# Performance work log

Hardware: AMD Instinct MI355X
Metric: run time of the kernel (lower is better)

## Reference

```python
import jax, jax.numpy as jnp
import numpy as np

B, S, D, H, DH = 8, 2048, 1024, 16, 64  # hidden_dim = H*DH


def _layer_norm(x, g, b, eps=1e-5):
    m = jnp.mean(x, axis=-1, keepdims=True)
    v = jnp.mean((x - m) ** 2, axis=-1, keepdims=True)
    return (x - m) / jnp.sqrt(v + eps) * g + b


def setup_inputs() -> dict:
    key = jax.random.key(0)
    ks = jax.random.split(key, 12)
    def xav(k, shape):
        # xavier_uniform with gain for relu = sqrt(2)
        fan_in, fan_out = shape[0], shape[1]
        a = np.sqrt(2.0) * np.sqrt(6.0 / (fan_in + fan_out))
        return jax.random.uniform(k, shape, jnp.float32, -a, a)
    return {
        "input_Q": jax.random.normal(ks[0], (B, S, D), jnp.float32),
        "input_K": jax.random.normal(ks[1], (B, S, D), jnp.float32),
        "input_V": jax.random.normal(ks[2], (B, S, D), jnp.float32),
        # weights stored [in, out] (torch Linear weight transposed)
        "Wq1": xav(ks[3], (D, DH // 2)),
        "Wq2": xav(ks[4], (DH // 2, DH * H)),
        "Wk1": xav(ks[5], (D, DH // 2)),
        "Wk2": xav(ks[6], (DH // 2, DH * H)),
        "Wv": xav(ks[7], (D, DH * H)),
        "Wfc": xav(ks[8], (D, D)),
        "A": xav(ks[9], (DH, DH)),
        "ln_g": jnp.ones((D,), jnp.float32),
        "ln_b": jnp.zeros((D,), jnp.float32),
    }


def reference(input_Q, input_K, input_V, Wq1, Wq2, Wk1, Wk2, Wv, Wfc, A, ln_g, ln_b):
    b, s, d = input_Q.shape
    residual = input_Q
    Q = (input_Q @ Wq1 @ Wq2).reshape(b, s, H, DH).transpose(0, 2, 1, 3)  # [B,H,S,dh]
    K = (input_K @ Wk1 @ Wk2).reshape(b, s, H, DH).transpose(0, 2, 1, 3)
    V = (input_V @ Wv).reshape(b, s, H, DH).transpose(0, 2, 1, 3)
    scale = 1.0 / np.sqrt(DH).astype(np.float32)
    # stage 1: scores[b,h,d,s] = sum_f A.T[d,f] K[b,h,s,f]
    scores_VV = jnp.einsum('fd,bhsf->bhds', A, K) * scale  # [B,H,dh,S]
    attn_VV = jax.nn.softmax(scores_VV, axis=-1)
    VV = jnp.einsum('bhds,bhsf->bhdf', attn_VV, V)  # [B,H,dh,dh]
    # stage 2: scores2[b,h,s,d] = sum_f Q[b,h,s,f] A[d,f]
    scores_VV2 = jnp.einsum('bhsf,df->bhsd', Q, A) * scale  # [B,H,S,dh]
    attn_VV2 = jax.nn.softmax(scores_VV2, axis=-1)
    VVV = jnp.einsum('bhsd,bhdf->bhsf', attn_VV2, VV)  # [B,H,S,dh]
    # faithful torch reshape: row-major flatten of [B,H,S,dh] into [B,S,H*dh]
    VVV = VVV.reshape(b, s, H * DH)
    outputs1 = _layer_norm(VVV + residual, ln_g, ln_b)
    outputs2 = outputs1 @ Wfc
    outputs = _layer_norm(outputs2 + outputs1, ln_g, ln_b)
    return (outputs, attn_VV)
```

## Files before the change

kernel.cpp:

```cpp
#include <hip/hip_runtime.h>
#include <hip/hip_bf16.h>
#include <stdint.h>

typedef __attribute__((ext_vector_type(4))) float f32x4;
typedef __attribute__((ext_vector_type(8))) short bf16x8;
typedef __attribute__((ext_vector_type(4))) unsigned short us4;
typedef __attribute__((ext_vector_type(8))) unsigned short us8;

static constexpr int Bb = 8, Ss = 2048, Dd = 1024, Hh = 16, DHh = 64;
static constexpr int Mm = Bb * Ss;
#define DEVI static __device__ __forceinline__

DEVI float bf2f(unsigned short u) {
  union { unsigned int i; float f; } v; v.i = ((unsigned int)u) << 16; return v.f;
}
DEVI unsigned short f2bf(float f) {
  union { float f; unsigned int i; } v; v.f = f;
  unsigned int r = v.i + 0x7FFFu + ((v.i >> 16) & 1u);
  return (unsigned short)(r >> 16);
}

__global__ __launch_bounds__(256) void k_transpose_w(const float* __restrict__ W,
                                                     unsigned short* __restrict__ WT) {
  __shared__ float tile[32][33];
  const int n0 = blockIdx.x * 32, k0 = blockIdx.y * 32;
  const int t = threadIdx.x, tr = t >> 5, tc = t & 31;
#pragma unroll
  for (int i = 0; i < 4; i++) {
    int r = tr + 8 * i;
    tile[r][tc] = W[(size_t)(k0 + r) * 1024 + n0 + tc];
  }
  __syncthreads();
#pragma unroll
  for (int i = 0; i < 4; i++) {
    int r = tr + 8 * i;
    WT[(size_t)(n0 + r) * 1024 + k0 + tc] = f2bf(tile[tc][r]);
  }
}

__global__ __launch_bounds__(256) void k_cvt(const float* __restrict__ x,
                                             unsigned short* __restrict__ y) {
  const int n4 = (Mm * Dd) / 4;
  for (int i = blockIdx.x * 256 + threadIdx.x; i < n4; i += gridDim.x * 256) {
    f32x4 v = ((const f32x4*)x)[i];
    us4 o = { f2bf(v.x), f2bf(v.y), f2bf(v.z), f2bf(v.w) };
    ((us4*)y)[i] = o;
  }
}

__global__ __launch_bounds__(256) void k_prep_at(const float* __restrict__ A,
                                                 unsigned short* __restrict__ At,
                                                 unsigned short* __restrict__ Ab) {
  int t = blockIdx.x * 256 + threadIdx.x;
  int d = t >> 6, f = t & 63;
  At[d * 64 + f] = f2bf(A[f * 64 + d]);
  Ab[t] = f2bf(A[t]);
}

__global__ __launch_bounds__(256) void k_qkmid(const float* __restrict__ inQ, const float* __restrict__ inK,
                                               const float* __restrict__ Wq1, const float* __restrict__ Wk1,
                                               float* __restrict__ Qmid, float* __restrict__ Kmid) {
  const float* in = blockIdx.y ? inK : inQ;
  const float* W  = blockIdx.y ? Wk1 : Wq1;
  float* outp     = blockIdx.y ? Kmid : Qmid;
  __shared__ float rows[8][1024];
  const int r0 = blockIdx.x * 8;
  const int t = threadIdx.x;
  const f32x4* src = (const f32x4*)(in + (size_t)r0 * 1024);
  f32x4* dstl = (f32x4*)rows;
#pragma unroll
  for (int i = 0; i < 8; i++) dstl[t + 256 * i] = src[t + 256 * i];
  __syncthreads();
  const int g = t >> 5, j = t & 31;
  float acc = 0.f;
#pragma unroll 8
  for (int k = 0; k < 1024; k++) acc += rows[g][k] * W[k * 32 + j];
  outp[(size_t)(r0 + g) * 32 + j] = acc;
}

__global__ __launch_bounds__(256) void k_qkexpand(const float* __restrict__ Qmid, const float* __restrict__ Kmid,
                                                  const float* __restrict__ Wq2, const float* __restrict__ Wk2,
                                                  unsigned short* __restrict__ Qp, unsigned short* __restrict__ Kp) {
  const float* mid = blockIdx.y ? Kmid : Qmid;
  const float* W   = blockIdx.y ? Wk2 : Wq2;
  unsigned short* outp = blockIdx.y ? Kp : Qp;
  __shared__ float sv[16][32];
  const int r0 = blockIdx.x * 16;
  const int t = threadIdx.x;
  ((float*)sv)[t]       = mid[(size_t)r0 * 32 + t];
  ((float*)sv)[t + 256] = mid[(size_t)r0 * 32 + t + 256];
  __syncthreads();
  const int c0 = t * 4;
  f32x4 acc[16];
#pragma unroll
  for (int ri = 0; ri < 16; ri++) acc[ri] = (f32x4){0.f, 0.f, 0.f, 0.f};
#pragma unroll
  for (int k = 0; k < 32; k++) {
    f32x4 w = *(const f32x4*)&W[k * 1024 + c0];
#pragma unroll
    for (int ri = 0; ri < 16; ri++) acc[ri] += sv[ri][k] * w;
  }
  const int h = c0 >> 6, f = c0 & 63;
#pragma unroll
  for (int ri = 0; ri < 16; ri++) {
    int r = r0 + ri;
    int b = r >> 11, s = r & 2047;
    us4 o = { f2bf(acc[ri].x), f2bf(acc[ri].y), f2bf(acc[ri].z), f2bf(acc[ri].w) };
    *(us4*)&outp[(((size_t)(b * 16 + h) * 2048) + s) * 64 + f] = o;
  }
}

__global__ __launch_bounds__(256) void k_transpose_bh(const unsigned short* __restrict__ src,
                                                      unsigned short* __restrict__ dst) {
  __shared__ unsigned short tile[64][72];
  const int bh = blockIdx.y, s0 = blockIdx.x * 64;
  const int t = threadIdx.x;
  {
    int sl = t >> 2, fc = (t & 3) * 16;
    const unsigned short* sp = src + ((size_t)bh * 2048 + s0 + sl) * 64 + fc;
    *(us8*)&tile[sl][fc]     = *(const us8*)sp;
    *(us8*)&tile[sl][fc + 8] = *(const us8*)(sp + 8);
  }
  __syncthreads();
  {
    int f = t >> 2, sc = (t & 3) * 16;
    unsigned short* dp = dst + ((size_t)bh * 64 + f) * 2048 + s0 + sc;
    us8 a, bq;
#pragma unroll
    for (int i = 0; i < 8; i++) a[i] = tile[sc + i][f];
#pragma unroll
    for (int i = 0; i < 8; i++) bq[i] = tile[sc + 8 + i][f];
    *(us8*)dp = a;
    *(us8*)(dp + 8) = bq;
  }
}

template <int EPI>
__global__ __launch_bounds__(256) void k_gemm(const unsigned short* __restrict__ Ag,
                                              const unsigned short* __restrict__ BTg,
                                              void* __restrict__ Cout) {
  __shared__ unsigned short As[128 * 64];
  __shared__ unsigned short Bs[128 * 64];
  const int m0 = blockIdx.y * 128, n0 = blockIdx.x * 128;
  const int t = threadIdx.x;
  const int w = t >> 6, l = t & 63;
  const int wr = w >> 1, wc = w & 1;
  const int g4 = l >> 4, l16 = l & 15;
  f32x4 acc[4][4];
#pragma unroll
  for (int i = 0; i < 4; i++)
#pragma unroll
    for (int jj = 0; jj < 4; jj++) acc[i][jj] = (f32x4){0.f, 0.f, 0.f, 0.f};

  const int srow = t >> 1, shalf = (t & 1) * 32;
  const us8* ga = (const us8*)(Ag  + (size_t)(m0 + srow) * 1024 + shalf);
  const us8* gb = (const us8*)(BTg + (size_t)(n0 + srow) * 1024 + shalf);
  const int swz = (srow & 7) << 4;
#pragma unroll 1
  for (int kt = 0; kt < 16; kt++) {
    __syncthreads();
#pragma unroll
    for (int c = 0; c < 4; c++) {
      int kb = (shalf + c * 8) * 2;
      *(us8*)&As[srow * 64 + ((kb ^ swz) >> 1)] = ga[c];
      *(us8*)&Bs[srow * 64 + ((kb ^ swz) >> 1)] = gb[c];
    }
    ga += 8; gb += 8;
    __syncthreads();
#pragma unroll
    for (int kk = 0; kk < 64; kk += 32) {
      bf16x8 af[4], bfr[4];
      const int kbyte = (kk + 8 * g4) * 2;
#pragma unroll
      for (int mt = 0; mt < 4; mt++) {
        int row = wr * 64 + mt * 16 + l16;
        af[mt] = *(const bf16x8*)&As[row * 64 + ((kbyte ^ ((row & 7) << 4)) >> 1)];
      }
#pragma unroll
      for (int nt = 0; nt < 4; nt++) {
        int row = wc * 64 + nt * 16 + l16;
        bfr[nt] = *(const bf16x8*)&Bs[row * 64 + ((kbyte ^ ((row & 7) << 4)) >> 1)];
      }
#pragma unroll
      for (int mt = 0; mt < 4; mt++)
#pragma unroll
        for (int nt = 0; nt < 4; nt++)
          acc[mt][nt] = __builtin_amdgcn_mfma_f32_16x16x32_bf16(af[mt], bfr[nt], acc[mt][nt], 0, 0, 0);
    }
  }
#pragma unroll
  for (int mt = 0; mt < 4; mt++)
#pragma unroll
    for (int nt = 0; nt < 4; nt++)
#pragma unroll
      for (int r = 0; r < 4; r++) {
        int m = m0 + wr * 64 + mt * 16 + g4 * 4 + r;
        int n = n0 + wc * 64 + nt * 16 + l16;
        float v = acc[mt][nt][r];
        if (EPI == 0) {
          int b = m >> 11, s = m & 2047, h = n >> 6, f = n & 63;
          ((unsigned short*)Cout)[(((size_t)(b * 16 + h) * 2048) + s) * 64 + f] = f2bf(v);
        } else {
          ((float*)Cout)[(size_t)m * 1024 + n] = v;
        }
      }
}

__global__ __launch_bounds__(512) void k_stage1m(const unsigned short* __restrict__ Kp,
                                                 const unsigned short* __restrict__ VpT,
                                                 const unsigned short* __restrict__ At,
                                                 float* __restrict__ attn_out,
                                                 float* __restrict__ VVn) {
  __shared__ unsigned short Ks[256 * 64];
  __shared__ unsigned short VTs[64 * 256];
  __shared__ unsigned short Ps[64 * 256];
  __shared__ float mred[512], lred[512], mfin[64], linv[64];
  const int bh = blockIdx.x;
  const int t = threadIdx.x;
  const int w = t >> 6, l = t & 63;
  const int l16 = l & 15, g4 = l >> 4;
  const unsigned short* kg = Kp  + (size_t)bh * 131072;
  const unsigned short* vg = VpT + (size_t)bh * 131072;

  bf16x8 bfr[4][2];
#pragma unroll
  for (int nt = 0; nt < 4; nt++)
#pragma unroll
    for (int ks = 0; ks < 2; ks++)
      bfr[nt][ks] = *(const bf16x8*)&At[(nt * 16 + l16) * 64 + ks * 32 + g4 * 8];

  float m4[4], l4[4];
#pragma unroll
  for (int nt = 0; nt < 4; nt++) { m4[nt] = -1e30f; l4[nt] = 0.f; }

  for (int st = 0; st < 8; st++) {
    __syncthreads();
#pragma unroll
    for (int i = 0; i < 4; i++) {
      int chunk = t + 512 * i;
      int row = chunk >> 3, fo = (chunk & 7) * 8;
      us8 v = *(const us8*)&kg[(size_t)(st * 256 + row) * 64 + fo];
      *(us8*)&Ks[row * 64 + (((fo * 2) ^ ((row & 7) << 4)) >> 1)] = v;
    }
    __syncthreads();
    f32x4 s_[2][4];
#pragma unroll
    for (int mt = 0; mt < 2; mt++)
#pragma unroll
      for (int nt = 0; nt < 4; nt++) s_[mt][nt] = (f32x4){0.f, 0.f, 0.f, 0.f};
#pragma unroll
    for (int mt = 0; mt < 2; mt++) {
      int ar = w * 32 + mt * 16 + l16;
#pragma unroll
      for (int ks = 0; ks < 2; ks++) {
        bf16x8 af = *(const bf16x8*)&Ks[ar * 64 + (((ks * 64 + g4 * 16) ^ ((ar & 7) << 4)) >> 1)];
#pragma unroll
        for (int nt = 0; nt < 4; nt++)
          s_[mt][nt] = __builtin_amdgcn_mfma_f32_16x16x32_bf16(af, bfr[nt][ks], s_[mt][nt], 0, 0, 0);
      }
    }
#pragma unroll
    for (int nt = 0; nt < 4; nt++) {
      float tm = s_[0][nt][0];
#pragma unroll
      for (int r = 1; r < 4; r++) tm = fmaxf(tm, s_[0][nt][r]);
#pragma unroll
      for (int r = 0; r < 4; r++) tm = fmaxf(tm, s_[1][nt][r]);
      tm *= 0.125f;
      float mn = fmaxf(m4[nt], tm);
      float sum = 0.f;
#pragma unroll
      for (int mt = 0; mt < 2; mt++)
#pragma unroll
        for (int r = 0; r < 4; r++) sum += __expf(s_[mt][nt][r] * 0.125f - mn);
      l4[nt] = l4[nt] * __expf(m4[nt] - mn) + sum;
      m4[nt] = mn;
    }
  }
#pragma unroll
  for (int nt = 0; nt < 4; nt++) {
#pragma unroll
    for (int off = 16; off < 64; off <<= 1) {
      float m2 = __shfl_xor(m4[nt], off);
      float l2 = __shfl_xor(l4[nt], off);
      float mn = fmaxf(m4[nt], m2);
      l4[nt] = l4[nt] * __expf(m4[nt] - mn) + l2 * __expf(m2 - mn);
      m4[nt] = mn;
    }
  }
  if (l < 16) {
#pragma unroll
    for (int nt = 0; nt < 4; nt++) {
      mred[w * 64 + nt * 16 + l] = m4[nt];
      lred[w * 64 + nt * 16 + l] = l4[nt];
    }
  }
  __syncthreads();
  if (w == 0) {
    float m = -1e30f;
#pragma unroll
    for (int wv = 0; wv < 8; wv++) m = fmaxf(m, mred[wv * 64 + l]);
    float ls = 0.f;
#pragma unroll
    for (int wv = 0; wv < 8; wv++) ls += lred[wv * 64 + l] * __expf(mred[wv * 64 + l] - m);
    mfin[l] = m;
    linv[l] = 1.f / ls;
  }

  f32x4 vv[2];
  vv[0] = (f32x4){0.f, 0.f, 0.f, 0.f};
  vv[1] = (f32x4){0.f, 0.f, 0.f, 0.f};
  const int mtv = w & 3, nbase = (w >> 2) * 2;
  float* aout = attn_out + (size_t)bh * 131072;
  for (int st = 0; st < 8; st++) {
    __syncthreads();
#pragma unroll
    for (int i = 0; i < 4; i++) {
      int chunk = t + 512 * i;
      {
        int row = chunk >> 3, fo = (chunk & 7) * 8;
        us8 v = *(const us8*)&kg[(size_t)(st * 256 + row) * 64 + fo];
        *(us8*)&Ks[row * 64 + (((fo * 2) ^ ((row & 7) << 4)) >> 1)] = v;
      }
      {
        int fr = chunk >> 5, so = (chunk & 31) * 8;
        us8 v = *(const us8*)&vg[(size_t)fr * 2048 + st * 256 + so];
        *(us8*)&VTs[fr * 256 + (((so * 2) ^ ((fr & 7) << 4)) >> 1)] = v;
      }
    }
    __syncthreads();
    f32x4 s_[2][4];
#pragma unroll
    for (int mt = 0; mt < 2; mt++)
#pragma unroll
      for (int nt = 0; nt < 4; nt++) s_[mt][nt] = (f32x4){0.f, 0.f, 0.f, 0.f};
#pragma unroll
    for (int mt = 0; mt < 2; mt++) {
      int ar = w * 32 + mt * 16 + l16;
#pragma unroll
      for (int ks = 0; ks < 2; ks++) {
        bf16x8 af = *(const bf16x8*)&Ks[ar * 64 + (((ks * 64 + g4 * 16) ^ ((ar & 7) << 4)) >> 1)];
#pragma unroll
        for (int nt = 0; nt < 4; nt++)
          s_[mt][nt] = __builtin_amdgcn_mfma_f32_16x16x32_bf16(af, bfr[nt][ks], s_[mt][nt], 0, 0, 0);
      }
    }
#pragma unroll
    for (int mt = 0; mt < 2; mt++) {
      int sg = w * 32 + mt * 16 + g4 * 4;
#pragma unroll
      for (int nt = 0; nt < 4; nt++) {
        int d = nt * 16 + l16;
        float mf = mfin[d], il = linv[d];
        f32x4 ev;
#pragma unroll
        for (int r = 0; r < 4; r++) ev[r] = __expf(s_[mt][nt][r] * 0.125f - mf);
        f32x4 av = ev * il;
        *(f32x4*)&aout[(size_t)d * 2048 + st * 256 + sg] = av;
        us4 pb = { f2bf(ev.x), f2bf(ev.y), f2bf(ev.z), f2bf(ev.w) };
        *(us4*)&Ps[d * 256 + (((sg * 2) ^ ((d & 7) << 4)) >> 1)] = pb;
      }
    }
    __syncthreads();
#pragma unroll
    for (int ks = 0; ks < 8; ks++) {
      int ar = mtv * 16 + l16;
      bf16x8 pa = *(const bf16x8*)&Ps[ar * 256 + (((ks * 64 + g4 * 16) ^ ((ar & 7) << 4)) >> 1)];
#pragma unroll
      for (int j = 0; j < 2; j++) {
        int fr = (nbase + j) * 16 + l16;
        bf16x8 vb = *(const bf16x8*)&VTs[fr * 256 + (((ks * 64 + g4 * 16) ^ ((fr & 7) << 4)) >> 1)];
        vv[j] = __builtin_amdgcn_mfma_f32_16x16x32_bf16(pa, vb, vv[j], 0, 0, 0);
      }
    }
  }
#pragma unroll
  for (int j = 0; j < 2; j++)
#pragma unroll
    for (int r = 0; r < 4; r++) {
      int d = mtv * 16 + g4 * 4 + r;
      int f = (nbase + j) * 16 + l16;
      VVn[(size_t)bh * 4096 + d * 64 + f] = vv[j][r] * linv[d];
    }
}

__global__ __launch_bounds__(512) void k_stage2m(const unsigned short* __restrict__ Qp,
                                                 const unsigned short* __restrict__ Ab,
                                                 const float* __restrict__ VVn,
                                                 float* __restrict__ X) {
  __shared__ unsigned short Qs[256 * 64];
  __shared__ unsigned short Ps[256 * 64];
  __shared__ unsigned short VVT[64 * 64];
  const int bh = blockIdx.y, b = bh >> 4, h = bh & 15;
  const int stile = blockIdx.x;
  const int t = threadIdx.x;
  const int w = t >> 6, l = t & 63;
  const int l16 = l & 15, g4 = l >> 4;

  bf16x8 abf[4][2];
#pragma unroll
  for (int nt = 0; nt < 4; nt++)
#pragma unroll
    for (int ks = 0; ks < 2; ks++)
      abf[nt][ks] = *(const bf16x8*)&Ab[(nt * 16 + l16) * 64 + ks * 32 + g4 * 8];

  for (int i = t; i < 4096; i += 512) {
    int d = i >> 6, f = i & 63;
    float v = VVn[(size_t)bh * 4096 + i];
    VVT[f * 64 + (((d * 2) ^ ((f & 7) << 4)) >> 1)] = f2bf(v);
  }
  const unsigned short* qg = Qp + (size_t)bh * 131072 + (size_t)stile * 256 * 64;
#pragma unroll
  for (int i = 0; i < 4; i++) {
    int chunk = t + 512 * i;
    int row = chunk >> 3, fo = (chunk & 7) * 8;
    us8 v = *(const us8*)&qg[row * 64 + fo];
    *(us8*)&Qs[row * 64 + (((fo * 2) ^ ((row & 7) << 4)) >> 1)] = v;
  }
  __syncthreads();

  f32x4 s_[2][4];
#pragma unroll
  for (int mt = 0; mt < 2; mt++)
#pragma unroll
    for (int nt = 0; nt < 4; nt++) s_[mt][nt] = (f32x4){0.f, 0.f, 0.f, 0.f};
#pragma unroll
  for (int mt = 0; mt < 2; mt++) {
    int ar = w * 32 + mt * 16 + l16;
#pragma unroll
    for (int ks = 0; ks < 2; ks++) {
      bf16x8 af = *(const bf16x8*)&Qs[ar * 64 + (((ks * 64 + g4 * 16) ^ ((ar & 7) << 4)) >> 1)];
#pragma unroll
      for (int nt = 0; nt < 4; nt++)
        s_[mt][nt] = __builtin_amdgcn_mfma_f32_16x16x32_bf16(af, abf[nt][ks], s_[mt][nt], 0, 0, 0);
    }
  }

#pragma unroll
  for (int mt = 0; mt < 2; mt++) {
    f32x4 mx;
#pragma unroll
    for (int r = 0; r < 4; r++) {
      float m = s_[mt][0][r];
#pragma unroll
      for (int nt = 1; nt < 4; nt++) m = fmaxf(m, s_[mt][nt][r]);
      mx[r] = m;
    }
#pragma unroll
    for (int off = 1; off < 16; off <<= 1)
#pragma unroll
      for (int r = 0; r < 4; r++) mx[r] = fmaxf(mx[r], __shfl_xor(mx[r], off));
    f32x4 ev[4], sm = (f32x4){0.f, 0.f, 0.f, 0.f};
#pragma unroll
    for (int nt = 0; nt < 4; nt++)
#pragma unroll
      for (int r = 0; r < 4; r++) {
        ev[nt][r] = __expf((s_[mt][nt][r] - mx[r]) * 0.125f);
        sm[r] += ev[nt][r];
      }
#pragma unroll
    for (int off = 1; off < 16; off <<= 1)
#pragma unroll
      for (int r = 0; r < 4; r++) sm[r] += __shfl_xor(sm[r], off);
    f32x4 inv;
#pragma unroll
    for (int r = 0; r < 4; r++) inv[r] = 1.f / sm[r];
#pragma unroll
    for (int nt = 0; nt < 4; nt++)
#pragma unroll
      for (int r = 0; r < 4; r++) {
        int row = w * 32 + mt * 16 + g4 * 4 + r;
        int d = nt * 16 + l16;
        Ps[row * 64 + (((d * 2) ^ ((row & 7) << 4)) >> 1)] = f2bf(ev[nt][r] * inv[r]);
      }
  }
  f32x4 o_[2][4];
#pragma unroll
  for (int mt = 0; mt < 2; mt++)
#pragma unroll
    for (int nt = 0; nt < 4; nt++) o_[mt][nt] = (f32x4){0.f, 0.f, 0.f, 0.f};
#pragma unroll
  for (int mt = 0; mt < 2; mt++) {
    int ar = w * 32 + mt * 16 + l16;
#pragma unroll
    for (int ks = 0; ks < 2; ks++) {
      bf16x8 pa = *(const bf16x8*)&Ps[ar * 64 + (((ks * 64 + g4 * 16) ^ ((ar & 7) << 4)) >> 1)];
#pragma unroll
      for (int nt = 0; nt < 4; nt++) {
        int fr = nt * 16 + l16;
        bf16x8 vb = *(const bf16x8*)&VVT[fr * 64 + (((ks * 64 + g4 * 16) ^ ((fr & 7) << 4)) >> 1)];
        o_[mt][nt] = __builtin_amdgcn_mfma_f32_16x16x32_bf16(pa, vb, o_[mt][nt], 0, 0, 0);
      }
    }
  }
#pragma unroll
  for (int mt = 0; mt < 2; mt++)
#pragma unroll
    for (int nt = 0; nt < 4; nt++)
#pragma unroll
      for (int r = 0; r < 4; r++) {
        int sl = stile * 256 + w * 32 + mt * 16 + g4 * 4 + r;
        int f = nt * 16 + l16;
        int jj = h * 128 + (sl >> 4);
        int cc = (sl & 15) * 64 + f;
        X[((size_t)(b * 2048 + jj)) * 1024 + cc] = o_[mt][nt][r];
      }
}

template <bool WB>
__global__ __launch_bounds__(256) void k_ln(const float* __restrict__ xa, const float* __restrict__ xb,
                                            const float* __restrict__ g, const float* __restrict__ bbv,
                                            float* __restrict__ outf, unsigned short* __restrict__ outb) {
  __shared__ float red[2][4];
  const size_t row = blockIdx.x;
  const int t = threadIdx.x;
  const int wv = t >> 6, l = t & 63;
  f32x4 va = ((const f32x4*)(xa + row * 1024))[t];
  f32x4 vb = ((const f32x4*)(xb + row * 1024))[t];
  f32x4 v = va + vb;
  float s = v.x + v.y + v.z + v.w;
  float q = v.x * v.x + v.y * v.y + v.z * v.z + v.w * v.w;
#pragma unroll
  for (int o = 1; o < 64; o <<= 1) { s += __shfl_xor(s, o); q += __shfl_xor(q, o); }
  if (l == 0) { red[0][wv] = s; red[1][wv] = q; }
  __syncthreads();
  s = red[0][0] + red[0][1] + red[0][2] + red[0][3];
  q = red[1][0] + red[1][1] + red[1][2] + red[1][3];
  const float mean = s * (1.f / 1024.f);
  const float var = q * (1.f / 1024.f) - mean * mean;
  const float rstd = rsqrtf(var + 1e-5f);
  f32x4 gg = ((const f32x4*)g)[t];
  f32x4 bv = ((const f32x4*)bbv)[t];
  f32x4 o;
  o.x = (v.x - mean) * rstd * gg.x + bv.x;
  o.y = (v.y - mean) * rstd * gg.y + bv.y;
  o.z = (v.z - mean) * rstd * gg.z + bv.z;
  o.w = (v.w - mean) * rstd * gg.w + bv.w;
  ((f32x4*)(outf + row * 1024))[t] = o;
  if (WB) {
    us4 ob = { f2bf(o.x), f2bf(o.y), f2bf(o.z), f2bf(o.w) };
    ((us4*)(outb + row * 1024))[t] = ob;
  }
}

extern "C" void kernel_launch(void* const* d_in, const int* in_sizes, int n_in,
                              void* d_out, int out_size, void* d_ws, size_t ws_size,
                              hipStream_t stream) {
  const float* inQ = (const float*)d_in[0];
  const float* inK = (const float*)d_in[1];
  const float* inV = (const float*)d_in[2];
  const float* Wq1 = (const float*)d_in[3];
  const float* Wq2 = (const float*)d_in[4];
  const float* Wk1 = (const float*)d_in[5];
  const float* Wk2 = (const float*)d_in[6];
  const float* Wv  = (const float*)d_in[7];
  const float* Wfc = (const float*)d_in[8];
  const float* Aw  = (const float*)d_in[9];
  const float* lng = (const float*)d_in[10];
  const float* lnb = (const float*)d_in[11];
  float* out = (float*)d_out;
  float* attn_out = out + (size_t)Mm * Dd;

  char* ws = (char*)d_ws;
  unsigned short* WvT  = (unsigned short*)(ws + 0ull);
  unsigned short* WfcT = (unsigned short*)(ws + 2097152ull);
  float* Qmid          = (float*)(ws + 4194304ull);
  float* Kmid          = (float*)(ws + 6291456ull);
  unsigned short* Qp   = (unsigned short*)(ws + 8388608ull);
  unsigned short* Kp   = (unsigned short*)(ws + 41943040ull);
  unsigned short* KpT  = (unsigned short*)(ws + 75497472ull);
  unsigned short* VpT  = (unsigned short*)(ws + 109051904ull);
  unsigned short* Vbf  = (unsigned short*)(ws + 142606336ull);
  unsigned short* Vp   = (unsigned short*)(ws + 176160768ull);
  float* VVn           = (float*)(ws + 209715200ull);
  unsigned short* Atb = (unsigned short*)(ws + 4194304ull);
  unsigned short* A2b = (unsigned short*)(ws + 4194304ull + 8192ull);
  float* o2  = (float*)(ws + 75497472ull);
  float* X   = (float*)(ws + 142606336ull);
  float* o1f = X;
  unsigned short* o1b = Kp;
  (void)KpT;

  k_transpose_w<<<dim3(32, 32), 256, 0, stream>>>(Wv, WvT);
  k_transpose_w<<<dim3(32, 32), 256, 0, stream>>>(Wfc, WfcT);
  k_cvt<<<dim3(4096), 256, 0, stream>>>(inV, Vbf);
  k_qkmid<<<dim3(2048, 2), 256, 0, stream>>>(inQ, inK, Wq1, Wk1, Qmid, Kmid);
  k_qkexpand<<<dim3(1024, 2), 256, 0, stream>>>(Qmid, Kmid, Wq2, Wk2, Qp, Kp);
  k_prep_at<<<dim3(16), 256, 0, stream>>>(Aw, Atb, A2b);
  k_gemm<0><<<dim3(8, 128), 256, 0, stream>>>(Vbf, WvT, (void*)Vp);
  k_transpose_bh<<<dim3(32, 128), 256, 0, stream>>>(Vp, VpT);
  k_stage1m<<<dim3(128), 512, 0, stream>>>(Kp, VpT, Atb, attn_out, VVn);
  k_stage2m<<<dim3(8, 128), 512, 0, stream>>>(Qp, A2b, VVn, X);
  k_ln<true><<<dim3(16384), 256, 0, stream>>>(X, inQ, lng, lnb, o1f, o1b);
  k_gemm<1><<<dim3(8, 128), 256, 0, stream>>>(o1b, WfcT, (void*)o2);
  k_ln<false><<<dim3(16384), 256, 0, stream>>>(o2, o1f, lng, lnb, out, nullptr);
}
```

Before: 781.9 us.

## Fold low-rank Q/K projections into effective weights and use bf16 MFMA GEMM

Precomputes W1@W2 as a single 1024x1024 effective weight (transposed, bf16) for Q and K. The Q and K projections then run on the existing bf16 tensor-core GEMM after converting the inputs to bf16. This replaces the two scalar fp32 kernels that did the 1024->32->1024 factorised projection. In exchange it does far more FLOPs (a full-rank GEMM instead of rank-32) and adds two extra conversion passes over the inputs, betting that MFMA throughput beats the slow scalar fp32 path. It also adds some bf16 rounding error.

Result: faster. 715.9 us (-8.4%).

```diff
diff --git a/kernel.cpp b/kernel.cpp
--- a/kernel.cpp
+++ b/kernel.cpp
@@ -35,6 +35,35 @@
   for (int i = 0; i < 4; i++) {
     int r = tr + 8 * i;
     WT[(size_t)(n0 + r) * 1024 + k0 + tc] = f2bf(tile[tc][r]);
+  }
+}
+
+__global__ __launch_bounds__(256) void k_weff(const float* __restrict__ W1, const float* __restrict__ W2,
+                                              unsigned short* __restrict__ WT) {
+  __shared__ float s1[64][33];
+  __shared__ float s2[32][64];
+  const int n0 = blockIdx.x * 64, k0 = blockIdx.y * 64;
+  const int t = threadIdx.x;
+#pragma unroll
+  for (int u = 0; u < 8; u++) {
+    int e = t * 8 + u;
+    s1[e >> 5][e & 31] = W1[k0 * 32 + e];
+  }
+  {
+    int e = t * 8;
+    const f32x4* src = (const f32x4*)&W2[(size_t)(e >> 6) * 1024 + n0 + (e & 63)];
+    *(f32x4*)&s2[e >> 6][e & 63] = src[0];
+    *(f32x4*)&s2[e >> 6][(e & 63) + 4] = src[1];
+  }
+  __syncthreads();
+  const int g = t >> 6, kL = t & 63;
+#pragma unroll
+  for (int i = 0; i < 16; i++) {
+    int nL = g * 16 + i;
+    float acc = 0.f;
+#pragma unroll
+    for (int j = 0; j < 32; j++) acc += s1[kL][j] * s2[j][nL];
+    WT[(size_t)(n0 + nL) * 1024 + k0 + kL] = f2bf(acc);
   }
 }
 
@@ -55,59 +84,6 @@
   int d = t >> 6, f = t & 63;
   At[d * 64 + f] = f2bf(A[f * 64 + d]);
   Ab[t] = f2bf(A[t]);
-}
-
-__global__ __launch_bounds__(256) void k_qkmid(const float* __restrict__ inQ, const float* __restrict__ inK,
-                                               const float* __restrict__ Wq1, const float* __restrict__ Wk1,
-                                               float* __restrict__ Qmid, float* __restrict__ Kmid) {
-  const float* in = blockIdx.y ? inK : inQ;
-  const float* W  = blockIdx.y ? Wk1 : Wq1;
-  float* outp     = blockIdx.y ? Kmid : Qmid;
-  __shared__ float rows[8][1024];
-  const int r0 = blockIdx.x * 8;
-  const int t = threadIdx.x;
-  const f32x4* src = (const f32x4*)(in + (size_t)r0 * 1024);
-  f32x4* dstl = (f32x4*)rows;
-#pragma unroll
-  for (int i = 0; i < 8; i++) dstl[t + 256 * i] = src[t + 256 * i];
-  __syncthreads();
-  const int g = t >> 5, j = t & 31;
-  float acc = 0.f;
-#pragma unroll 8
-  for (int k = 0; k < 1024; k++) acc += rows[g][k] * W[k * 32 + j];
-  outp[(size_t)(r0 + g) * 32 + j] = acc;
-}
-
-__global__ __launch_bounds__(256) void k_qkexpand(const float* __restrict__ Qmid, const float* __restrict__ Kmid,
-                                                  const float* __restrict__ Wq2, const float* __restrict__ Wk2,
-                                                  unsigned short* __restrict__ Qp, unsigned short* __restrict__ Kp) {
-  const float* mid = blockIdx.y ? Kmid : Qmid;
-  const float* W   = blockIdx.y ? Wk2 : Wq2;
-  unsigned short* outp = blockIdx.y ? Kp : Qp;
-  __shared__ float sv[16][32];
-  const int r0 = blockIdx.x * 16;
-  const int t = threadIdx.x;
-  ((float*)sv)[t]       = mid[(size_t)r0 * 32 + t];
-  ((float*)sv)[t + 256] = mid[(size_t)r0 * 32 + t + 256];
-  __syncthreads();
-  const int c0 = t * 4;
-  f32x4 acc[16];
-#pragma unroll
-  for (int ri = 0; ri < 16; ri++) acc[ri] = (f32x4){0.f, 0.f, 0.f, 0.f};
-#pragma unroll
-  for (int k = 0; k < 32; k++) {
-    f32x4 w = *(const f32x4*)&W[k * 1024 + c0];
-#pragma unroll
-    for (int ri = 0; ri < 16; ri++) acc[ri] += sv[ri][k] * w;
-  }
-  const int h = c0 >> 6, f = c0 & 63;
-#pragma unroll
-  for (int ri = 0; ri < 16; ri++) {
-    int r = r0 + ri;
-    int b = r >> 11, s = r & 2047;
-    us4 o = { f2bf(acc[ri].x), f2bf(acc[ri].y), f2bf(acc[ri].z), f2bf(acc[ri].w) };
-    *(us4*)&outp[(((size_t)(b * 16 + h) * 2048) + s) * 64 + f] = o;
-  }
 }
 
 __global__ __launch_bounds__(256) void k_transpose_bh(const unsigned short* __restrict__ src,
@@ -562,33 +538,37 @@
   float* attn_out = out + (size_t)Mm * Dd;
 
   char* ws = (char*)d_ws;
-  unsigned short* WvT  = (unsigned short*)(ws + 0ull);
-  unsigned short* WfcT = (unsigned short*)(ws + 2097152ull);
-  float* Qmid          = (float*)(ws + 4194304ull);
-  float* Kmid          = (float*)(ws + 6291456ull);
-  unsigned short* Qp   = (unsigned short*)(ws + 8388608ull);
-  unsigned short* Kp   = (unsigned short*)(ws + 41943040ull);
-  unsigned short* KpT  = (unsigned short*)(ws + 75497472ull);
-  unsigned short* VpT  = (unsigned short*)(ws + 109051904ull);
-  unsigned short* Vbf  = (unsigned short*)(ws + 142606336ull);
-  unsigned short* Vp   = (unsigned short*)(ws + 176160768ull);
-  float* VVn           = (float*)(ws + 209715200ull);
-  unsigned short* Atb = (unsigned short*)(ws + 4194304ull);
-  unsigned short* A2b = (unsigned short*)(ws + 4194304ull + 8192ull);
-  float* o2  = (float*)(ws + 75497472ull);
-  float* X   = (float*)(ws + 142606336ull);
-  float* o1f = X;
-  unsigned short* o1b = Kp;
-  (void)KpT;
+  unsigned short* WvT    = (unsigned short*)(ws + 0ull);
+  unsigned short* WfcT   = (unsigned short*)(ws + 2097152ull);
+  unsigned short* WeffqT = (unsigned short*)(ws + 4194304ull);
+  unsigned short* WeffkT = (unsigned short*)(ws + 6291456ull);
+  unsigned short* Qp     = (unsigned short*)(ws + 8388608ull);
+  unsigned short* Kp     = (unsigned short*)(ws + 41943040ull);
+  float* o2              = (float*)(ws + 75497472ull);
+  unsigned short* Atb    = (unsigned short*)(ws + 75497472ull);
+  unsigned short* A2b    = (unsigned short*)(ws + 75497472ull + 8192ull);
+  unsigned short* VpT    = (unsigned short*)(ws + 109051904ull);
+  unsigned short* Vbf    = (unsigned short*)(ws + 142606336ull);
+  unsigned short* Qbf    = (unsigned short*)(ws + 142606336ull);
+  float* X               = (float*)(ws + 142606336ull);
+  float* o1f             = X;
+  unsigned short* Vp     = (unsigned short*)(ws + 176160768ull);
+  unsigned short* Kbf    = (unsigned short*)(ws + 176160768ull);
+  float* VVn             = (float*)(ws + 209715200ull);
+  unsigned short* o1b    = Kp;
 
   k_transpose_w<<<dim3(32, 32), 256, 0, stream>>>(Wv, WvT);
   k_transpose_w<<<dim3(32, 32), 256, 0, stream>>>(Wfc, WfcT);
+  k_weff<<<dim3(16, 16), 256, 0, stream>>>(Wq1, Wq2, WeffqT);
+  k_weff<<<dim3(16, 16), 256, 0, stream>>>(Wk1, Wk2, WeffkT);
+  k_prep_at<<<dim3(16), 256, 0, stream>>>(Aw, Atb, A2b);
   k_cvt<<<dim3(4096), 256, 0, stream>>>(inV, Vbf);
-  k_qkmid<<<dim3(2048, 2), 256, 0, stream>>>(inQ, inK, Wq1, Wk1, Qmid, Kmid);
-  k_qkexpand<<<dim3(1024, 2), 256, 0, stream>>>(Qmid, Kmid, Wq2, Wk2, Qp, Kp);
-  k_prep_at<<<dim3(16), 256, 0, stream>>>(Aw, Atb, A2b);
   k_gemm<0><<<dim3(8, 128), 256, 0, stream>>>(Vbf, WvT, (void*)Vp);
   k_transpose_bh<<<dim3(32, 128), 256, 0, stream>>>(Vp, VpT);
+  k_cvt<<<dim3(4096), 256, 0, stream>>>(inQ, Qbf);
+  k_cvt<<<dim3(4096), 256, 0, stream>>>(inK, Kbf);
+  k_gemm<0><<<dim3(8, 128), 256, 0, stream>>>(Qbf, WeffqT, (void*)Qp);
+  k_gemm<0><<<dim3(8, 128), 256, 0, stream>>>(Kbf, WeffkT, (void*)Kp);
   k_stage1m<<<dim3(128), 512, 0, stream>>>(Kp, VpT, Atb, attn_out, VVn);
   k_stage2m<<<dim3(8, 128), 512, 0, stream>>>(Qp, A2b, VVn, X);
   k_ln<true><<<dim3(16384), 256, 0, stream>>>(X, inQ, lng, lnb, o1f, o1b);
```
